# Kernel tuning notes

Hardware: AMD Instinct MI355X
Metric: run time of the kernel (lower is better)

Reference implementation:

```python
import jax, jax.numpy as jnp
import numpy as np

N_NODES = 100000
N_EDGES = 1600000  # directed, src < dst; to_undirected doubles them
N_GRAPHS = 128
D_IN, D_H, D_FC, N_CLS = 128, 64, 32, 10


def setup_inputs() -> dict:
    key = jax.random.key(0)
    ks = jax.random.split(key, 12)
    x = jax.random.normal(ks[0], (N_NODES, D_IN), dtype=jnp.float32)
    # edges with src < dst so concatenating the flipped copy yields the undirected set
    r = jax.random.randint(ks[1], (2, N_EDGES), 0, N_NODES, dtype=jnp.int64)
    src = jnp.minimum(r[0], r[1])
    dst = jnp.maximum(r[0], r[1])
    dst = jnp.where(src == dst, (dst + 1) % N_NODES, dst)  # avoid pre-existing self loops
    edge_index = jnp.stack([src, dst])
    batch = jnp.sort(jax.random.randint(ks[2], (N_NODES,), 0, N_GRAPHS, dtype=jnp.int64))
    sc = lambda f: 1.0 / jnp.sqrt(jnp.float32(f))
    return {
        "x": x,
        "edge_index": edge_index,
        "batch": batch,
        "W_in": jax.random.normal(ks[3], (D_IN, D_H), jnp.float32) * sc(D_IN),
        "b_in": jnp.zeros((D_H,), jnp.float32),
        "W1": jax.random.normal(ks[4], (D_H, D_H), jnp.float32) * sc(D_H),
        "b1": jnp.zeros((D_H,), jnp.float32),
        "W2": jax.random.normal(ks[5], (D_H, D_H), jnp.float32) * sc(D_H),
        "b2": jnp.zeros((D_H,), jnp.float32),
        "Wf1": jax.random.normal(ks[6], (D_H, D_FC), jnp.float32) * sc(D_H),
        "bf1": jnp.zeros((D_FC,), jnp.float32),
        "Wf2": jax.random.normal(ks[7], (D_FC, N_CLS), jnp.float32) * sc(D_FC),
        "bf2": jnp.zeros((N_CLS,), jnp.float32),
    }


def _gcn_conv(x, W, b, src, dst, dinv, n_nodes):
    # GCNConv: x' = D^{-1/2}(A+I)D^{-1/2} (xW) + b, dinv = deg^{-1/2} incl. self loops
    xw = x @ W
    norm = (dinv[src] * dinv[dst])[:, None]              # [E,1]
    agg = jax.ops.segment_sum(xw[src] * norm, dst, num_segments=n_nodes)
    agg = agg + xw * (dinv * dinv)[:, None]              # self-loop term
    return agg + b


def reference(x, edge_index, batch, W_in, b_in, W1, b1, W2, b2, Wf1, bf1, Wf2, bf2):
    n = x.shape[0]
    # to_undirected: append reversed edges (inputs have src<dst, so no dup dirs)
    src = jnp.concatenate([edge_index[0], edge_index[1]])
    dst = jnp.concatenate([edge_index[1], edge_index[0]])
    # degree including self loop
    deg = 1.0 + jax.ops.segment_sum(jnp.ones_like(dst, dtype=x.dtype), dst, num_segments=n)
    dinv = jax.lax.rsqrt(deg)

    h = jax.nn.relu(x @ W_in + b_in)
    h = jax.nn.relu(_gcn_conv(h, W1, b1, src, dst, dinv, n))
    h = jax.nn.relu(_gcn_conv(h, W2, b2, src, dst, dinv, n))

    # global_mean_pool over graph ids
    sums = jax.ops.segment_sum(h, batch, num_segments=N_GRAPHS)
    cnts = jax.ops.segment_sum(jnp.ones((n,), h.dtype), batch, num_segments=N_GRAPHS)
    pooled = sums / jnp.maximum(cnts, 1.0)[:, None]

    g = jax.nn.relu(pooled @ Wf1 + bf1)
    logits = g @ Wf2 + bf2
    return jax.nn.log_softmax(logits, axis=1)
```

## Files before the change

kernel.cpp:

```cpp
#include <hip/hip_runtime.h>
#include <hip/hip_fp16.h>
#include <math.h>

constexpr int DG  = 128;
constexpr int DIN = 128;
constexpr int DH  = 64;
constexpr int DFC = 32;
constexpr int DC  = 10;
constexpr int CAP    = 80;
constexpr int NB     = 2048;
constexpr int ABLK   = 256;
constexpr int SCAP   = 2048;
constexpr int MAXNPB = 52;

__global__ __launch_bounds__(256) void k_hist(const int* __restrict__ src,
                                              const int* __restrict__ dst,
                                              int* __restrict__ histT,
                                              int E, int EPB, int NPB) {
    __shared__ int h[NB];
    for (int i = threadIdx.x; i < NB; i += 256) h[i] = 0;
    __syncthreads();
    int e0 = blockIdx.x * EPB, e1 = min(e0 + EPB, E);
    for (int i = e0 + threadIdx.x; i < e1; i += 256) {
        int u = src[i], v = dst[i];
        atomicAdd(&h[v / NPB], 1);
        atomicAdd(&h[u / NPB], 1);
    }
    __syncthreads();
    for (int i = threadIdx.x; i < NB; i += 256)
        histT[(size_t)i * ABLK + blockIdx.x] = h[i];
}

__global__ __launch_bounds__(256) void k_expand(const int* __restrict__ histT,
                                                int* __restrict__ baseT,
                                                int* __restrict__ ecnt,
                                                float* __restrict__ sums,
                                                int* __restrict__ cnts) {
    __shared__ int s[256];
    int b = blockIdx.x, t = threadIdx.x;
    int v = histT[(size_t)b * ABLK + t];
    s[t] = v;
    __syncthreads();
    for (int o = 1; o < 256; o <<= 1) {
        int tv = (t >= o) ? s[t - o] : 0;
        __syncthreads();
        s[t] += tv;
        __syncthreads();
    }
    int incl = s[t];
    baseT[(size_t)b * ABLK + t] = b * SCAP + incl - v;
    if (t == 255) ecnt[b] = min(incl, SCAP);
    int gid = b * 256 + t;
    if (gid < DG * DH) sums[gid] = 0.0f;
    if (gid < DG) cnts[gid] = 0;
}

__global__ __launch_bounds__(256) void k_binplace(const int* __restrict__ src,
                                                  const int* __restrict__ dst,
                                                  const int* __restrict__ baseT,
                                                  int* __restrict__ staging,
                                                  int E, int EPB, int NPB) {
    __shared__ int lcnt[NB];
    __shared__ int lbase[NB];
    int blk = blockIdx.x;
    for (int i = threadIdx.x; i < NB; i += 256) {
        lcnt[i]  = 0;
        lbase[i] = baseT[(size_t)i * ABLK + blk];
    }
    __syncthreads();
    int e0 = blk * EPB, e1 = min(e0 + EPB, E);
    for (int i = e0 + threadIdx.x; i < e1; i += 256) {
        int u = src[i], v = dst[i];
        int bv = v / NPB, bu = u / NPB;
        int rv = atomicAdd(&lcnt[bv], 1);
        int sv = lbase[bv] + rv;
        if (sv < (bv + 1) * SCAP) staging[sv] = ((v - bv * NPB) << 17) | u;
        int ru = atomicAdd(&lcnt[bu], 1);
        int su = lbase[bu] + ru;
        if (su < (bu + 1) * SCAP) staging[su] = ((u - bu * NPB) << 17) | v;
    }
}

__global__ __launch_bounds__(256) void k_rows(const int* __restrict__ staging,
                                              const int* __restrict__ ecnt,
                                              int* __restrict__ adj,
                                              int* __restrict__ cnt,
                                              float* __restrict__ dinv,
                                              int N, int NPB) {
    __shared__ int rows[MAXNPB * CAP];
    __shared__ int cur[MAXNPB];
    int b = blockIdx.x;
    int nbase = b * NPB;
    int nn = min(NPB, N - nbase);
    if (nn <= 0) return;
    for (int i = threadIdx.x; i < nn; i += 256) cur[i] = 0;
    __syncthreads();
    int s0 = b * SCAP, s1 = s0 + ecnt[b];
    for (int i = s0 + threadIdx.x; i < s1; i += 256) {
        int e  = staging[i];
        int vl = e >> 17;
        int u  = e & 0x1FFFF;
        int p  = atomicAdd(&cur[vl], 1);
        if (p < CAP) rows[vl * CAP + p] = u;
    }
    __syncthreads();
    for (int s = threadIdx.x; s < nn * CAP; s += 256) {
        int node = s / CAP, p = s - node * CAP;
        if (p < min(cur[node], CAP))
            adj[(size_t)(nbase + node) * CAP + p] = rows[s];
    }
    for (int i = threadIdx.x; i < nn; i += 256) {
        int c = cur[i];
        cnt[nbase + i]  = c;
        dinv[nbase + i] = rsqrtf(1.0f + (float)c);
    }
}

__global__ __launch_bounds__(256) void k_lin2(const float* __restrict__ x,
                                              const float* __restrict__ Wi,
                                              const float* __restrict__ bi,
                                              const float* __restrict__ W1,
                                              const float* __restrict__ dinv,
                                              __half* __restrict__ out, int n) {
    __shared__ float sx[16 * DIN];
    __shared__ float part[16 * 4 * DH];
    __shared__ float sh[16 * DH];
    int t = threadIdx.x;
    int lane = t & 63, w = t >> 6;
    float wreg[32];
#pragma unroll
    for (int i = 0; i < 32; i++) wreg[i] = Wi[(w * 32 + i) * DH + lane];
    float bb = bi[lane];
    int tile = blockIdx.x * 16;
    const float4* xsrc = (const float4*)(x + (size_t)tile * DIN);
    float4* sx4 = (float4*)sx;
    sx4[t]       = xsrc[t];
    sx4[t + 256] = xsrc[t + 256];
    __syncthreads();
#pragma unroll 1
    for (int r = 0; r < 16; r++) {
        const float4* xr = (const float4*)(sx + r * DIN + w * 32);
        float a0 = 0.f, a1 = 0.f, a2 = 0.f, a3 = 0.f;
#pragma unroll
        for (int q = 0; q < 8; q++) {
            float4 xv = xr[q];
            a0 = fmaf(xv.x, wreg[q * 4 + 0], a0);
            a1 = fmaf(xv.y, wreg[q * 4 + 1], a1);
            a2 = fmaf(xv.z, wreg[q * 4 + 2], a2);
            a3 = fmaf(xv.w, wreg[q * 4 + 3], a3);
        }
        part[(r * 4 + w) * DH + lane] = (a0 + a1) + (a2 + a3);
    }
    __syncthreads();
#pragma unroll
    for (int q = 0; q < 4; q++) {
        int r = w * 4 + q;
        float s = part[(r * 4 + 0) * DH + lane] + part[(r * 4 + 1) * DH + lane]
                + part[(r * 4 + 2) * DH + lane] + part[(r * 4 + 3) * DH + lane] + bb;
        sh[r * DH + lane] = fmaxf(s, 0.0f);
    }
    float w1[64];
#pragma unroll
    for (int i = 0; i < 64; i++) w1[i] = W1[i * DH + lane];
    __syncthreads();
#pragma unroll
    for (int q = 0; q < 4; q++) {
        int r = w * 4 + q;
        const float4* hr = (const float4*)(sh + r * DH);
        float a0 = 0.f, a1 = 0.f, a2 = 0.f, a3 = 0.f;
#pragma unroll
        for (int p = 0; p < 16; p++) {
            float4 xv = hr[p];
            a0 = fmaf(xv.x, w1[p * 4 + 0], a0);
            a1 = fmaf(xv.y, w1[p * 4 + 1], a1);
            a2 = fmaf(xv.z, w1[p * 4 + 2], a2);
            a3 = fmaf(xv.w, w1[p * 4 + 3], a3);
        }
        float dv = dinv[tile + r];
        out[(size_t)(tile + r) * DH + lane] = __float2half(((a0 + a1) + (a2 + a3)) * dv);
    }
}

__global__ __launch_bounds__(256) void k_mm64(const __half* __restrict__ h,
                                              const float* __restrict__ W,
                                              const float* __restrict__ dinv,
                                              __half* __restrict__ out, int n) {
    __shared__ float sx[16 * DH];
    int t = threadIdx.x, lane = t & 63, w = t >> 6;
    float wreg[64];
#pragma unroll
    for (int i = 0; i < 64; i++) wreg[i] = W[i * DH + lane];
    int tile = blockIdx.x * 16;
    {
        const __half2* hsrc = (const __half2*)(h + (size_t)tile * DH);
        float2* sx2 = (float2*)sx;
        sx2[t * 2]     = __half22float2(hsrc[t * 2]);
        sx2[t * 2 + 1] = __half22float2(hsrc[t * 2 + 1]);
    }
    __syncthreads();
#pragma unroll
    for (int q = 0; q < 4; q++) {
        int r = w * 4 + q;
        const float4* xr = (const float4*)(sx + r * DH);
        float a0 = 0.f, a1 = 0.f, a2 = 0.f, a3 = 0.f;
#pragma unroll
        for (int p = 0; p < 16; p++) {
            float4 xv = xr[p];
            a0 = fmaf(xv.x, wreg[p * 4 + 0], a0);
            a1 = fmaf(xv.y, wreg[p * 4 + 1], a1);
            a2 = fmaf(xv.z, wreg[p * 4 + 2], a2);
            a3 = fmaf(xv.w, wreg[p * 4 + 3], a3);
        }
        float dv = dinv[tile + r];
        out[(size_t)(tile + r) * DH + lane] = __float2half(((a0 + a1) + (a2 + a3)) * dv);
    }
}

__global__ __launch_bounds__(256) void k_gather(const int* __restrict__ cnt,
                                                const int* __restrict__ adj,
                                                const __half2* __restrict__ xws,
                                                const float* __restrict__ dinv,
                                                const float* __restrict__ b,
                                                __half* __restrict__ out, int n) {
    int lane = threadIdx.x & 63;
    int v    = blockIdx.x * 4 + (threadIdx.x >> 6);
    if (v >= n) return;
    int half_id = lane >> 5, fp = lane & 31;
    int len = min(cnt[v], CAP);
    const int* row = adj + (size_t)v * CAP;
    int idx = 0;
    if (lane < len) idx = row[lane];
    int len64 = min(len, 64);
    const char* xb = (const char*)xws;
    int fpo = fp << 2;
    float ax = 0.f, ay = 0.f;
    int k = half_id;
    for (; k + 14 < len64; k += 16) {
        int u0 = __shfl(idx, k);
        int u1 = __shfl(idx, k + 2);
        int u2 = __shfl(idx, k + 4);
        int u3 = __shfl(idx, k + 6);
        int u4 = __shfl(idx, k + 8);
        int u5 = __shfl(idx, k + 10);
        int u6 = __shfl(idx, k + 12);
        int u7 = __shfl(idx, k + 14);
        __half2 h0 = *(const __half2*)(xb + ((u0 << 7) | fpo));
        __half2 h1 = *(const __half2*)(xb + ((u1 << 7) | fpo));
        __half2 h2 = *(const __half2*)(xb + ((u2 << 7) | fpo));
        __half2 h3 = *(const __half2*)(xb + ((u3 << 7) | fpo));
        h0 = __hadd2(h0, *(const __half2*)(xb + ((u4 << 7) | fpo)));
        h1 = __hadd2(h1, *(const __half2*)(xb + ((u5 << 7) | fpo)));
        h2 = __hadd2(h2, *(const __half2*)(xb + ((u6 << 7) | fpo)));
        h3 = __hadd2(h3, *(const __half2*)(xb + ((u7 << 7) | fpo)));
        float2 f0 = __half22float2(h0);
        float2 f1 = __half22float2(h1);
        float2 f2 = __half22float2(h2);
        float2 f3 = __half22float2(h3);
        ax += (f0.x + f1.x) + (f2.x + f3.x);
        ay += (f0.y + f1.y) + (f2.y + f3.y);
    }
    for (; k < len64; k += 2) {
        int u0 = __shfl(idx, k);
        float2 f0 = __half22float2(*(const __half2*)(xb + ((u0 << 7) | fpo)));
        ax += f0.x; ay += f0.y;
    }
    for (int j = 64 + half_id; j < len; j += 2) {
        float2 f0 = __half22float2(xws[(size_t)row[j] * 32 + fp]);
        ax += f0.x; ay += f0.y;
    }
    ax += __shfl_xor(ax, 32);
    ay += __shfl_xor(ay, 32);
    if (half_id == 0) {
        float2 s  = __half22float2(xws[(size_t)v * 32 + fp]);
        float  dv = dinv[v];
        float2 bb = ((const float2*)b)[fp];
        __half2 o = __floats2half2_rn(fmaxf(dv * (ax + s.x) + bb.x, 0.0f),
                                      fmaxf(dv * (ay + s.y) + bb.y, 0.0f));
        ((__half2*)out)[(size_t)v * 32 + fp] = o;
    }
}

__global__ __launch_bounds__(256) void k_pool(const __half* __restrict__ h,
                                              const int* __restrict__ batch,
                                              float* __restrict__ sums,
                                              int* __restrict__ cnts, int n) {
    int lane = threadIdx.x & 63;
    int w    = blockIdx.x * 4 + (threadIdx.x >> 6);
    int start = w * 64;
    if (start >= n) return;
    int end  = min(start + 64, n);
    int curg = batch[start];
    float acc = 0.f;
    int   c   = 0;
    for (int node = start; node < end; node++) {
        int g = batch[node];
        if (g != curg) {
            atomicAdd(&sums[curg * DH + lane], acc);
            if (lane == 0) atomicAdd(&cnts[curg], c);
            acc = 0.f; c = 0; curg = g;
        }
        acc += __half2float(h[(size_t)node * DH + lane]);
        c++;
    }
    atomicAdd(&sums[curg * DH + lane], acc);
    if (lane == 0) atomicAdd(&cnts[curg], c);
}

__global__ __launch_bounds__(64) void k_head(const float* __restrict__ sums,
                                             const int* __restrict__ cnts,
                                             const float* __restrict__ Wf1,
                                             const float* __restrict__ bf1,
                                             const float* __restrict__ Wf2,
                                             const float* __restrict__ bf2,
                                             float* __restrict__ out) {
    int g = blockIdx.x, lane = threadIdx.x;
    float cnt    = (float)max(cnts[g], 1);
    float pooled = sums[g * DH + lane] / cnt;
    float acc = (lane < DFC) ? bf1[lane] : 0.f;
    for (int k = 0; k < DH; k++) {
        float pk = __shfl(pooled, k);
        if (lane < DFC) acc = fmaf(pk, Wf1[k * DFC + lane], acc);
    }
    float gv = fmaxf(acc, 0.f);
    float acc2 = (lane < DC) ? bf2[lane] : 0.f;
    for (int k = 0; k < DFC; k++) {
        float gk = __shfl(gv, k);
        if (lane < DC) acc2 = fmaf(gk, Wf2[k * DC + lane], acc2);
    }
    float v = (lane < DC) ? acc2 : -INFINITY;
    float m = v;
    for (int o = 8; o; o >>= 1) m = fmaxf(m, __shfl_xor(m, o));
    float e = (lane < DC) ? expf(v - m) : 0.f;
    float s = e;
    for (int o = 8; o; o >>= 1) s += __shfl_xor(s, o);
    if (lane < DC) out[g * DC + lane] = v - m - logf(s);
}

extern "C" void kernel_launch(void* const* d_in, const int* in_sizes, int n_in,
                              void* d_out, int out_size, void* d_ws, size_t ws_size,
                              hipStream_t stream) {
    const float* x    = (const float*)d_in[0];
    const int*   ei   = (const int*)d_in[1];
    const int*   batch= (const int*)d_in[2];
    const float* W_in = (const float*)d_in[3];
    const float* b_in = (const float*)d_in[4];
    const float* W1   = (const float*)d_in[5];
    const float* b1   = (const float*)d_in[6];
    const float* W2   = (const float*)d_in[7];
    const float* b2   = (const float*)d_in[8];
    const float* Wf1  = (const float*)d_in[9];
    const float* bf1  = (const float*)d_in[10];
    const float* Wf2  = (const float*)d_in[11];
    const float* bf2  = (const float*)d_in[12];
    float* out = (float*)d_out;

    const int E = in_sizes[1] / 2;
    const int N = in_sizes[0] / DIN;
    const int* src = ei;
    const int* dst = ei + E;

    const int NPB = (N + NB - 1) / NB;
    const int NBU = (N + NPB - 1) / NPB;
    const int EPB = (E + ABLK - 1) / ABLK;

    char* ws = (char*)d_ws;
    size_t off = 0;
    auto alloc = [&](size_t bytes) -> void* {
        void* p = ws + off;
        off = (off + bytes + 255) & ~(size_t)255;
        return p;
    };
    int*    cnt     = (int*)   alloc((size_t)N * 4);
    float*  dinv    = (float*) alloc((size_t)N * 4);
    int*    adj     = (int*)   alloc((size_t)N * CAP * 4);
    int*    histT   = (int*)   alloc((size_t)ABLK * NB * 4);
    int*    baseT   = (int*)   alloc((size_t)ABLK * NB * 4);
    int*    ecnt    = (int*)   alloc((size_t)NB * 4);
    int*    staging = (int*)   alloc((size_t)NB * SCAP * 4);
    __half* hA      = (__half*)alloc((size_t)N * DH * 2);
    __half* hX      = (__half*)alloc((size_t)N * DH * 2);
    float*  sums    = (float*) alloc((size_t)DG * DH * 4);
    int*    cnts    = (int*)   alloc((size_t)DG * 4);

    k_hist<<<ABLK, 256, 0, stream>>>(src, dst, histT, E, EPB, NPB);
    k_expand<<<NB, 256, 0, stream>>>(histT, baseT, ecnt, sums, cnts);
    k_binplace<<<ABLK, 256, 0, stream>>>(src, dst, baseT, staging, E, EPB, NPB);
    k_rows<<<NBU, 256, 0, stream>>>(staging, ecnt, adj, cnt, dinv, N, NPB);

    k_lin2<<<N / 16, 256, 0, stream>>>(x, W_in, b_in, W1, dinv, hX, N);

    k_gather<<<(N + 3) / 4, 256, 0, stream>>>(cnt, adj, (const __half2*)hX, dinv, b1, hA, N);

    k_mm64<<<N / 16, 256, 0, stream>>>(hA, W2, dinv, hX, N);
    k_gather<<<(N + 3) / 4, 256, 0, stream>>>(cnt, adj, (const __half2*)hX, dinv, b2, hA, N);

    int pw = (N + 63) / 64;
    k_pool<<<(pw + 3) / 4, 256, 0, stream>>>(hA, batch, sums, cnts, N);

    k_head<<<DG, 64, 0, stream>>>(sums, cnts, Wf1, bf1, Wf2, bf2, out);
}
```

Before: 318.5 us.

## Use fp16 MFMA for dense layers with pre-transposed half-precision weights

```diff
diff --git a/kernel.cpp b/kernel.cpp
--- a/kernel.cpp
+++ b/kernel.cpp
@@ -12,6 +12,14 @@
 constexpr int ABLK   = 256;
 constexpr int SCAP   = 2048;
 constexpr int MAXNPB = 52;
+
+typedef _Float16 f16;
+typedef f16  f16x8 __attribute__((ext_vector_type(8)));
+typedef float f32x4 __attribute__((ext_vector_type(4)));
+
+__device__ __forceinline__ int swz(int row, int byte_in_row) {
+    return row * 128 + (byte_in_row ^ ((row & 7) << 4));
+}
 
 __global__ __launch_bounds__(256) void k_hist(const int* __restrict__ src,
                                               const int* __restrict__ dst,
@@ -116,103 +124,105 @@
     }
 }
 
+__global__ __launch_bounds__(256) void k_wprep(const float* __restrict__ Wi,
+                                               const float* __restrict__ W1,
+                                               const float* __restrict__ W2,
+                                               f16* __restrict__ WiT,
+                                               f16* __restrict__ W1T,
+                                               f16* __restrict__ W2T) {
+    int t = blockIdx.x * 256 + threadIdx.x;
+    int stride = gridDim.x * 256;
+    for (int i = t; i < DH * DIN; i += stride) {
+        int c = i >> 7, k = i & 127;
+        WiT[i] = (f16)Wi[k * DH + c];
+    }
+    for (int i = t; i < DH * DH; i += stride) {
+        int c = i >> 6, k = i & 63;
+        W1T[i] = (f16)W1[k * DH + c];
+        W2T[i] = (f16)W2[k * DH + c];
+    }
+}
+
 __global__ __launch_bounds__(256) void k_lin2(const float* __restrict__ x,
-                                              const float* __restrict__ Wi,
+                                              const f16* __restrict__ WiT,
                                               const float* __restrict__ bi,
-                                              const float* __restrict__ W1,
+                                              const f16* __restrict__ W1T,
                                               const float* __restrict__ dinv,
                                               __half* __restrict__ out, int n) {
-    __shared__ float sx[16 * DIN];
-    __shared__ float part[16 * 4 * DH];
-    __shared__ float sh[16 * DH];
-    int t = threadIdx.x;
-    int lane = t & 63, w = t >> 6;
-    float wreg[32];
-#pragma unroll
-    for (int i = 0; i < 32; i++) wreg[i] = Wi[(w * 32 + i) * DH + lane];
-    float bb = bi[lane];
-    int tile = blockIdx.x * 16;
-    const float4* xsrc = (const float4*)(x + (size_t)tile * DIN);
-    float4* sx4 = (float4*)sx;
-    sx4[t]       = xsrc[t];
-    sx4[t + 256] = xsrc[t + 256];
-    __syncthreads();
-#pragma unroll 1
-    for (int r = 0; r < 16; r++) {
-        const float4* xr = (const float4*)(sx + r * DIN + w * 32);
-        float a0 = 0.f, a1 = 0.f, a2 = 0.f, a3 = 0.f;
-#pragma unroll
-        for (int q = 0; q < 8; q++) {
-            float4 xv = xr[q];
-            a0 = fmaf(xv.x, wreg[q * 4 + 0], a0);
-            a1 = fmaf(xv.y, wreg[q * 4 + 1], a1);
-            a2 = fmaf(xv.z, wreg[q * 4 + 2], a2);
-            a3 = fmaf(xv.w, wreg[q * 4 + 3], a3);
+    __shared__ f16 h0[4 * 16 * 64];
+    int t = threadIdx.x, lane = t & 63, w = t >> 6;
+    int rb = blockIdx.x * 64 + w * 16;
+    if (rb >= n) return;
+    int lr = lane & 15;
+    int lg = lane >> 4;
+    f16x8 a[4];
+    const float* xrow = x + (size_t)(rb + lr) * DIN + lg * 8;
+#pragma unroll
+    for (int k0 = 0; k0 < 4; k0++) {
+        float4 f0 = *(const float4*)(xrow + k0 * 32);
+        float4 f1 = *(const float4*)(xrow + k0 * 32 + 4);
+        a[k0][0] = (f16)f0.x; a[k0][1] = (f16)f0.y; a[k0][2] = (f16)f0.z; a[k0][3] = (f16)f0.w;
+        a[k0][4] = (f16)f1.x; a[k0][5] = (f16)f1.y; a[k0][6] = (f16)f1.z; a[k0][7] = (f16)f1.w;
+    }
+    char* hwb = (char*)(h0 + w * 16 * 64);
+#pragma unroll
+    for (int cb = 0; cb < 4; cb++) {
+        f32x4 acc = {0.f, 0.f, 0.f, 0.f};
+        const f16* wt = WiT + (cb * 16 + lr) * DIN + lg * 8;
+#pragma unroll
+        for (int k0 = 0; k0 < 4; k0++) {
+            f16x8 bf = *(const f16x8*)(wt + k0 * 32);
+            acc = __builtin_amdgcn_mfma_f32_16x16x32_f16(a[k0], bf, acc, 0, 0, 0);
         }
-        part[(r * 4 + w) * DH + lane] = (a0 + a1) + (a2 + a3);
-    }
-    __syncthreads();
-#pragma unroll
-    for (int q = 0; q < 4; q++) {
-        int r = w * 4 + q;
-        float s = part[(r * 4 + 0) * DH + lane] + part[(r * 4 + 1) * DH + lane]
-                + part[(r * 4 + 2) * DH + lane] + part[(r * 4 + 3) * DH + lane] + bb;
-        sh[r * DH + lane] = fmaxf(s, 0.0f);
-    }
-    float w1[64];
-#pragma unroll
-    for (int i = 0; i < 64; i++) w1[i] = W1[i * DH + lane];
-    __syncthreads();
-#pragma unroll
-    for (int q = 0; q < 4; q++) {
-        int r = w * 4 + q;
-        const float4* hr = (const float4*)(sh + r * DH);
-        float a0 = 0.f, a1 = 0.f, a2 = 0.f, a3 = 0.f;
-#pragma unroll
-        for (int p = 0; p < 16; p++) {
-            float4 xv = hr[p];
-            a0 = fmaf(xv.x, w1[p * 4 + 0], a0);
-            a1 = fmaf(xv.y, w1[p * 4 + 1], a1);
-            a2 = fmaf(xv.z, w1[p * 4 + 2], a2);
-            a3 = fmaf(xv.w, w1[p * 4 + 3], a3);
+        float bv = bi[cb * 16 + lr];
+#pragma unroll
+        for (int r = 0; r < 4; r++) {
+            int row = lg * 4 + r;
+            *(f16*)(hwb + swz(row, (cb * 16 + lr) * 2)) = (f16)fmaxf(acc[r] + bv, 0.0f);
         }
-        float dv = dinv[tile + r];
-        out[(size_t)(tile + r) * DH + lane] = __float2half(((a0 + a1) + (a2 + a3)) * dv);
+    }
+    f16x8 a2[2];
+#pragma unroll
+    for (int k0 = 0; k0 < 2; k0++)
+        a2[k0] = *(const f16x8*)(hwb + swz(lr, k0 * 64 + lg * 16));
+    float dv[4];
+#pragma unroll
+    for (int r = 0; r < 4; r++) dv[r] = dinv[rb + lg * 4 + r];
+#pragma unroll
+    for (int cb = 0; cb < 4; cb++) {
+        f32x4 acc = {0.f, 0.f, 0.f, 0.f};
+        const f16* wt = W1T + (cb * 16 + lr) * DH + lg * 8;
+        acc = __builtin_amdgcn_mfma_f32_16x16x32_f16(a2[0], *(const f16x8*)(wt), acc, 0, 0, 0);
+        acc = __builtin_amdgcn_mfma_f32_16x16x32_f16(a2[1], *(const f16x8*)(wt + 32), acc, 0, 0, 0);
+#pragma unroll
+        for (int r = 0; r < 4; r++)
+            out[(size_t)(rb + lg * 4 + r) * DH + cb * 16 + lr] = __float2half(acc[r] * dv[r]);
     }
 }
 
 __global__ __launch_bounds__(256) void k_mm64(const __half* __restrict__ h,
-                                              const float* __restrict__ W,
+                                              const f16* __restrict__ WT,
                                               const float* __restrict__ dinv,
                                               __half* __restrict__ out, int n) {
-    __shared__ float sx[16 * DH];
     int t = threadIdx.x, lane = t & 63, w = t >> 6;
-    float wreg[64];
-#pragma unroll
-    for (int i = 0; i < 64; i++) wreg[i] = W[i * DH + lane];
-    int tile = blockIdx.x * 16;
-    {
-        const __half2* hsrc = (const __half2*)(h + (size_t)tile * DH);
-        float2* sx2 = (float2*)sx;
-        sx2[t * 2]     = __half22float2(hsrc[t * 2]);
-        sx2[t * 2 + 1] = __half22float2(hsrc[t * 2 + 1]);
-    }
-    __syncthreads();
-#pragma unroll
-    for (int q = 0; q < 4; q++) {
-        int r = w * 4 + q;
-        const float4* xr = (const float4*)(sx + r * DH);
-        float a0 = 0.f, a1 = 0.f, a2 = 0.f, a3 = 0.f;
-#pragma unroll
-        for (int p = 0; p < 16; p++) {
-            float4 xv = xr[p];
-            a0 = fmaf(xv.x, wreg[p * 4 + 0], a0);
-            a1 = fmaf(xv.y, wreg[p * 4 + 1], a1);
-            a2 = fmaf(xv.z, wreg[p * 4 + 2], a2);
-            a3 = fmaf(xv.w, wreg[p * 4 + 3], a3);
-        }
-        float dv = dinv[tile + r];
-        out[(size_t)(tile + r) * DH + lane] = __float2half(((a0 + a1) + (a2 + a3)) * dv);
+    int rb = blockIdx.x * 64 + w * 16;
+    if (rb >= n) return;
+    int lr = lane & 15, lg = lane >> 4;
+    const f16* hp = (const f16*)h + (size_t)(rb + lr) * DH + lg * 8;
+    f16x8 a0 = *(const f16x8*)(hp);
+    f16x8 a1 = *(const f16x8*)(hp + 32);
+    float dv[4];
+#pragma unroll
+    for (int r = 0; r < 4; r++) dv[r] = dinv[rb + lg * 4 + r];
+#pragma unroll
+    for (int cb = 0; cb < 4; cb++) {
+        const f16* wt = WT + (cb * 16 + lr) * DH + lg * 8;
+        f32x4 acc = {0.f, 0.f, 0.f, 0.f};
+        acc = __builtin_amdgcn_mfma_f32_16x16x32_f16(a0, *(const f16x8*)(wt), acc, 0, 0, 0);
+        acc = __builtin_amdgcn_mfma_f32_16x16x32_f16(a1, *(const f16x8*)(wt + 32), acc, 0, 0, 0);
+#pragma unroll
+        for (int r = 0; r < 4; r++)
+            out[(size_t)(rb + lg * 4 + r) * DH + cb * 16 + lr] = __float2half(acc[r] * dv[r]);
     }
 }
 
@@ -381,17 +391,22 @@
     __half* hX      = (__half*)alloc((size_t)N * DH * 2);
     float*  sums    = (float*) alloc((size_t)DG * DH * 4);
     int*    cnts    = (int*)   alloc((size_t)DG * 4);
+    f16*    WiT     = (f16*)   alloc((size_t)DH * DIN * 2);
+    f16*    W1T     = (f16*)   alloc((size_t)DH * DH * 2);
+    f16*    W2T     = (f16*)   alloc((size_t)DH * DH * 2);
+
+    k_wprep<<<32, 256, 0, stream>>>(W_in, W1, W2, WiT, W1T, W2T);
 
     k_hist<<<ABLK, 256, 0, stream>>>(src, dst, histT, E, EPB, NPB);
     k_expand<<<NB, 256, 0, stream>>>(histT, baseT, ecnt, sums, cnts);
     k_binplace<<<ABLK, 256, 0, stream>>>(src, dst, baseT, staging, E, EPB, NPB);
     k_rows<<<NBU, 256, 0, stream>>>(staging, ecnt, adj, cnt, dinv, N, NPB);
 
-    k_lin2<<<N / 16, 256, 0, stream>>>(x, W_in, b_in, W1, dinv, hX, N);
+    k_lin2<<<(N + 63) / 64, 256, 0, stream>>>(x, WiT, b_in, W1T, dinv, hX, N);
 
     k_gather<<<(N + 3) / 4, 256, 0, stream>>>(cnt, adj, (const __half2*)hX, dinv, b1, hA, N);
 
-    k_mm64<<<N / 16, 256, 0, stream>>>(hA, W2, dinv, hX, N);
+    k_mm64<<<(N + 63) / 64, 256, 0, stream>>>(hA, W2T, dinv, hX, N);
     k_gather<<<(N + 3) / 4, 256, 0, stream>>>(cnt, adj, (const __half2*)hX, dinv, b2, hA, N);
 
     int pw = (N + 63) / 64;
```

Result: faster. 289.9 us (-9.0%).
